# Kernel tuning notes

Measured on AMD Instinct MI355X. Metric: run time of the kernel, lower is better.

Reference implementation:

```python
import jax, jax.numpy as jnp
import numpy as np

B, S, D, F = 4, 2048, 1024, 4096

def setup_inputs() -> dict:
    key = jax.random.key(0)
    ks = jax.random.split(key, 6)
    return {
        "x": jax.random.normal(ks[0], (B, S, D), jnp.float32),
        "Qw": jax.random.normal(ks[1], (D, D), jnp.float32) / 40,
        "Kw": jax.random.normal(ks[2], (D, D), jnp.float32) / 40,
        "Vw": jax.random.normal(ks[3], (D, D), jnp.float32) / 40,
        "w1": jax.random.normal(ks[4], (D, F), jnp.float32) / 40,
        "b1": jnp.zeros((F,), jnp.float32),
        "w2": jax.random.normal(ks[5], (F, D), jnp.float32) / 40,
        "b2": jnp.zeros((D,), jnp.float32),
        "gamma1": jnp.ones((D,), jnp.float32),
        "beta1": jnp.zeros((D,), jnp.float32),
        "gamma2": jnp.ones((D,), jnp.float32),
        "beta2": jnp.zeros((D,), jnp.float32),
    }

def _layernorm(x, gamma, beta):
    num = x - jnp.mean(x, axis=-1, keepdims=True)
    den = jnp.sqrt(jnp.var(x, axis=-1, keepdims=True) + 1e-05)
    return gamma * (num / den) + beta

def _attention(x, Qw, Kw, Vw):
    Q, K, V = x @ Qw, x @ Kw, x @ Vw
    d = x.shape[-1]
    s = x.shape[-2]
    mask = jnp.where(jnp.tril(jnp.ones((s, s))) == 0, -jnp.inf, 0.0)
    scores = Q @ jnp.swapaxes(K, -1, -2) / jnp.sqrt(d) + mask
    return jax.nn.softmax(scores, axis=-1) @ V

def reference(x, Qw, Kw, Vw, w1, b1, w2, b2, gamma1, beta1, gamma2, beta2):
    x = x + _attention(_layernorm(x, gamma1, beta1), Qw, Kw, Vw)
    h = _layernorm(x, gamma2, beta2)
    x = x + (jax.nn.relu(h @ w1 + b1) @ w2 + b2)
    return x
```

## Files before the change

### kernel.cpp

```cpp
#include <hip/hip_runtime.h>
#include <hip/hip_bf16.h>

#define B_ 4
#define S_ 2048
#define D_ 1024
#define F_ 4096

typedef short bf16x8 __attribute__((ext_vector_type(8)));
typedef float f32x4 __attribute__((ext_vector_type(4)));

static __device__ __forceinline__ unsigned short f2bf(float f) {
    union { float f; unsigned int u; } v; v.f = f;
    unsigned int u = v.u + 0x7FFF + ((v.u >> 16) & 1);
    return (unsigned short)(u >> 16);
}
static __device__ __forceinline__ float bf2f(unsigned short u) {
    union { unsigned int u; float f; } v; v.u = ((unsigned int)u) << 16;
    return v.f;
}

typedef const __attribute__((address_space(1))) unsigned int* gp_t;
typedef __attribute__((address_space(3))) unsigned int* lp_t;
static __device__ __forceinline__ void gld16(const unsigned short* g, unsigned short* l) {
    __builtin_amdgcn_global_load_lds((gp_t)g, (lp_t)l, 16, 0, 0);
}

#define WAIT_VM8()   __builtin_amdgcn_s_waitcnt(0x0F78)
#define WAIT_VM6()   __builtin_amdgcn_s_waitcnt(0x0F76)
#define WAIT_VM0()   __builtin_amdgcn_s_waitcnt(0x0F70)
#define WAIT_LGKM0() __builtin_amdgcn_s_waitcnt(0xC07F)

__global__ __launch_bounds__(256) void k_transpose_f32_bf16(
    const float* __restrict__ in, unsigned short* __restrict__ out, int R, int C) {
    __shared__ float t[32][33];
    int c0 = blockIdx.x * 32, r0 = blockIdx.y * 32;
    int x = threadIdx.x, y = threadIdx.y;
#pragma unroll
    for (int i = 0; i < 4; i++)
        t[y + 8 * i][x] = in[(size_t)(r0 + y + 8 * i) * C + c0 + x];
    __syncthreads();
#pragma unroll
    for (int i = 0; i < 4; i++)
        out[(size_t)(c0 + y + 8 * i) * R + r0 + x] = f2bf(t[x][y + 8 * i]);
}

__global__ __launch_bounds__(256) void k_transpose_w3(
    const float* __restrict__ Qw, const float* __restrict__ Kw, const float* __restrict__ Vw,
    unsigned short* __restrict__ out) {
    __shared__ float t[32][33];
    int z = blockIdx.z;
    const float* in = (z == 0) ? Qw : (z == 1) ? Kw : Vw;
    out += (size_t)z * D_ * D_;
    int c0 = blockIdx.x * 32, r0 = blockIdx.y * 32;
    int x = threadIdx.x, y = threadIdx.y;
#pragma unroll
    for (int i = 0; i < 4; i++)
        t[y + 8 * i][x] = in[(size_t)(r0 + y + 8 * i) * D_ + c0 + x];
    __syncthreads();
#pragma unroll
    for (int i = 0; i < 4; i++)
        out[(size_t)(c0 + y + 8 * i) * D_ + r0 + x] = f2bf(t[x][y + 8 * i]);
}

__global__ __launch_bounds__(256) void k_layernorm(
    const float* __restrict__ x, const float* __restrict__ gamma,
    const float* __restrict__ beta, unsigned short* __restrict__ out) {
    int row = blockIdx.x;
    int t = threadIdx.x;
    const float* xr = x + (size_t)row * D_;
    float4 v = ((const float4*)xr)[t];
    float s = v.x + v.y + v.z + v.w;
    float q = v.x * v.x + v.y * v.y + v.z * v.z + v.w * v.w;
#pragma unroll
    for (int off = 32; off; off >>= 1) {
        s += __shfl_down(s, off);
        q += __shfl_down(q, off);
    }
    __shared__ float ls[4], lq[4];
    int wv = t >> 6;
    if ((t & 63) == 0) { ls[wv] = s; lq[wv] = q; }
    __syncthreads();
    if (t == 0) {
        float S = ls[0] + ls[1] + ls[2] + ls[3];
        float Q = lq[0] + lq[1] + lq[2] + lq[3];
        float mean = S * (1.0f / D_);
        float var = Q * (1.0f / D_) - mean * mean;
        ls[0] = mean; lq[0] = rsqrtf(var + 1e-5f);
    }
    __syncthreads();
    float mean = ls[0], rstd = lq[0];
    float4 g = ((const float4*)gamma)[t];
    float4 b = ((const float4*)beta)[t];
    ushort4 o;
    o.x = f2bf(g.x * (v.x - mean) * rstd + b.x);
    o.y = f2bf(g.y * (v.y - mean) * rstd + b.y);
    o.z = f2bf(g.z * (v.z - mean) * rstd + b.z);
    o.w = f2bf(g.w * (v.w - mean) * rstd + b.w);
    ((ushort4*)(out + (size_t)row * D_))[t] = o;
}

__global__ __launch_bounds__(256) void k_softmax(unsigned short* __restrict__ sp) {
    int r = blockIdx.x;
    int i = r & (S_ - 1);
    unsigned short* row = sp + (size_t)r * S_;
    int t = threadIdx.x;
    int valid = i + 1;
    int wlim = (valid + 127) & ~127;
    bf16x8 v8 = {};
    if (t * 8 < valid) v8 = *(const bf16x8*)(row + t * 8);
    float vals[8];
    float mx = -1e30f;
#pragma unroll
    for (int k = 0; k < 8; k++) {
        int j = t * 8 + k;
        vals[k] = (j < valid) ? bf2f((unsigned short)v8[k]) : -1e30f;
        mx = fmaxf(mx, vals[k]);
    }
#pragma unroll
    for (int off = 32; off; off >>= 1) mx = fmaxf(mx, __shfl_xor(mx, off));
    __shared__ float red[4];
    if ((t & 63) == 0) red[t >> 6] = mx;
    __syncthreads();
    mx = fmaxf(fmaxf(red[0], red[1]), fmaxf(red[2], red[3]));
    __syncthreads();
    float e[8];
    float sum = 0.f;
#pragma unroll
    for (int k = 0; k < 8; k++) {
        int j = t * 8 + k;
        e[k] = (j < valid) ? __expf(vals[k] - mx) : 0.f;
        sum += e[k];
    }
#pragma unroll
    for (int off = 32; off; off >>= 1) sum += __shfl_xor(sum, off);
    if ((t & 63) == 0) red[t >> 6] = sum;
    __syncthreads();
    sum = red[0] + red[1] + red[2] + red[3];
    float inv = 1.0f / sum;
    if (t * 8 < wlim) {
        bf16x8 o8;
#pragma unroll
        for (int k = 0; k < 8; k++) o8[k] = (short)f2bf(e[k] * inv);
        *(bf16x8*)(row + t * 8) = o8;
    }
}

template <int EPI>
__global__ __launch_bounds__(256) void k_gemm_bt(
    const unsigned short* __restrict__ A, const unsigned short* __restrict__ Bt,
    void* __restrict__ Cv, const float* __restrict__ bias, const float* __restrict__ res,
    int K, int lda, int ldb, int ldc,
    long long sA, long long sB, long long sC, float scale, int klimit, int swz) {
    int bn, bm, z;
    if (swz > 0) {
        int GN = gridDim.x, GM = gridDim.y;
        int L = blockIdx.x + GN * (blockIdx.y + GM * blockIdx.z);
        int rows = gridDim.y * gridDim.z;
        int xcd = L & 7;
        int s = L >> 3;
        int bng = GN / swz;
        int rpg = rows * swz / 8;
        int xg = xcd % swz, yg = xcd / swz;
        int bnl = s % bng;
        int rl = s / bng;
        int row = yg * rpg + rl;
        bn = xg * bng + bnl;
        bm = row % GM;
        z = row / GM;
    } else {
        bn = blockIdx.x; bm = blockIdx.y; z = blockIdx.z;
    }
    if (EPI == 1 && bn > bm) return;
    A += (long long)z * sA;
    Bt += (long long)z * sB;
    long long coff = (long long)z * sC;
    float* Cf = (float*)Cv;
    unsigned short* Cb = (unsigned short*)Cv;

    __shared__ unsigned short As[2][2][128 * 32];
    __shared__ unsigned short Bs[2][2][128 * 32];

    int t = threadIdx.x;
    int l = t & 63, w = t >> 6;
    int wm = (w & 1) * 64, wn = (w >> 1) * 64;
    int lr = l & 15, lq = l >> 4;

    f32x4 acc[4][4];
#pragma unroll
    for (int i = 0; i < 4; i++)
#pragma unroll
        for (int j = 0; j < 4; j++) acc[i][j] = (f32x4){0.f, 0.f, 0.f, 0.f};

    int kend = K;
    if (klimit) { int ke = (bm + 1) * 128; kend = ke < K ? ke : K; }

    int sr = l >> 2;
    int sc = (l & 3) * 8;
    const unsigned short* gA0 = A + (size_t)(bm * 128 + w * 32 + sr) * lda + sc;
    const unsigned short* gA1 = gA0 + (size_t)16 * lda;
    const unsigned short* gB0 = Bt + (size_t)(bn * 128 + w * 32 + sr) * ldb + sc;
    const unsigned short* gB1 = gB0 + (size_t)16 * ldb;

    auto stage = [&](int buf, int k0) {
#pragma unroll
        for (int kc = 0; kc < 2; kc++) {
            int kk = k0 + kc * 32;
            gld16(gA0 + kk, &As[buf][kc][(w * 32) * 32]);
            gld16(gA1 + kk, &As[buf][kc][(w * 32 + 16) * 32]);
            gld16(gB0 + kk, &Bs[buf][kc][(w * 32) * 32]);
            gld16(gB1 + kk, &Bs[buf][kc][(w * 32 + 16) * 32]);
        }
    };

    int NB = kend >> 6;
    stage(0, 0);
    for (int it = 0; it < NB; it++) {
        int cur = it & 1;
        if (it + 1 < NB) {
            stage(1 - cur, (it + 1) * 64);
            WAIT_VM8();
        } else {
            WAIT_VM0();
        }
        __builtin_amdgcn_s_barrier();
#pragma unroll
        for (int kc = 0; kc < 2; kc++) {
            bf16x8 af[4], bf[4];
#pragma unroll
            for (int i = 0; i < 4; i++)
                af[i] = *(const bf16x8*)(&As[cur][kc][(wm + i * 16 + lr) * 32 + lq * 8]);
#pragma unroll
            for (int j = 0; j < 4; j++)
                bf[j] = *(const bf16x8*)(&Bs[cur][kc][(wn + j * 16 + lr) * 32 + lq * 8]);
#pragma unroll
            for (int i = 0; i < 4; i++)
#pragma unroll
                for (int j = 0; j < 4; j++)
                    acc[i][j] = __builtin_amdgcn_mfma_f32_16x16x32_bf16(af[i], bf[j], acc[i][j], 0, 0, 0);
        }
        __builtin_amdgcn_s_barrier();
    }

#pragma unroll
    for (int i = 0; i < 4; i++) {
        int mbase = bm * 128 + wm + i * 16 + lq * 4;
#pragma unroll
        for (int j = 0; j < 4; j++) {
            int n = bn * 128 + wn + j * 16 + lr;
#pragma unroll
            for (int r = 0; r < 4; r++) {
                int m = mbase + r;
                float v = acc[i][j][r];
                long long idx = coff + (long long)m * ldc + n;
                if (EPI == 0) {
                    Cb[idx] = f2bf(v);
                } else if (EPI == 1) {
                    Cb[idx] = f2bf(v * scale);
                } else if (EPI == 2) {
                    Cf[idx] = v + res[idx];
                } else if (EPI == 3) {
                    float u = v + bias[n];
                    Cb[idx] = f2bf(u > 0.f ? u : 0.f);
                } else {
                    Cf[idx] = v + bias[n] + res[idx];
                }
            }
        }
    }
}

template <int EPI>
__global__ __launch_bounds__(512, 2) void k_gemm256(
    const unsigned short* __restrict__ A, const unsigned short* __restrict__ Bt,
    void* __restrict__ Cv, const float* __restrict__ bias, const float* __restrict__ res,
    int K, int lda, int ldb, int ldc,
    long long sA, long long sB, long long sC, float scale, int klimit) {
    int bn = blockIdx.x, bm = blockIdx.y, z = blockIdx.z;
    if (EPI == 1 && bn > bm) return;
    A += (long long)z * sA;
    Bt += (long long)z * sB;
    long long coff = (long long)z * sC;
    float* Cf = (float*)Cv;
    unsigned short* Cb = (unsigned short*)Cv;

    __shared__ unsigned short As[2][2][128 * 64];
    __shared__ unsigned short Bs[2][2][128 * 64];

    int t = threadIdx.x;
    int l = t & 63, w = t >> 6;
    int wmh = w >> 2;
    int wnh = (w >> 1) & 1;
    int bnl = (w & 1) * 64;
    int lr = l & 15, lq = l >> 4;
    int rx = (lr & 7) << 3;
    int c0 = lq * 8;

    f32x4 acc[8][4];
#pragma unroll
    for (int i = 0; i < 8; i++)
#pragma unroll
        for (int j = 0; j < 4; j++) acc[i][j] = (f32x4){0.f, 0.f, 0.f, 0.f};

    int kend = K;
    if (klimit) { int ke = (bm + 1) * 256; kend = ke < K ? ke : K; }
    int NB = kend >> 6;

    int grow = l >> 3;
    int gcol = ((l & 7) * 8) ^ (((l >> 3) & 7) << 3);
    const unsigned short* gA = A + (size_t)(bm * 256 + w * 16 + grow) * lda + gcol;
    const unsigned short* gB = Bt + (size_t)(bn * 256 + w * 16 + grow) * ldb + gcol;

    auto stageA = [&](int buf, int half, int k0) {
        const unsigned short* g = gA + (size_t)(half * 128) * lda + k0;
        unsigned short* s = &As[buf][half][(w * 16) * 64];
        gld16(g, s);
        gld16(g + (size_t)8 * lda, s + 8 * 64);
    };
    auto stageB = [&](int buf, int half, int k0) {
        const unsigned short* g = gB + (size_t)(half * 128) * ldb + k0;
        unsigned short* s = &Bs[buf][half][(w * 16) * 64];
        gld16(g, s);
        gld16(g + (size_t)8 * ldb, s + 8 * 64);
    };

    stageA(0, 0, 0); stageA(0, 1, 0);
    stageB(0, 0, 0); stageB(0, 1, 0);
    int kp = (NB > 1) ? 64 : 0;
    stageB(1, 0, kp); stageB(1, 1, kp); stageA(1, 0, kp);
    WAIT_VM6();
    __builtin_amdgcn_s_barrier();

    bf16x8 aF0[2][4], aF1[2][4], bF[2][4];

    for (int j = 0; j < NB; j++) {
        int b = j & 1;
        int k1 = ((j + 1 < NB) ? (j + 1) : (NB - 1)) << 6;
        int k2 = ((j + 2 < NB) ? (j + 2) : (NB - 1)) << 6;
        const unsigned short* Ah = &As[b][wmh][0];
        const unsigned short* Bh = &Bs[b][wnh][0];

#pragma unroll
        for (int kc = 0; kc < 2; kc++) {
#pragma unroll
            for (int f = 0; f < 4; f++)
                bF[kc][f] = *(const bf16x8*)(Bh + (bnl + f * 16 + lr) * 64 + ((kc * 32 + c0) ^ rx));
#pragma unroll
            for (int f = 0; f < 4; f++)
                aF0[kc][f] = *(const bf16x8*)(Ah + (f * 16 + lr) * 64 + ((kc * 32 + c0) ^ rx));
        }
        stageA(b ^ 1, 1, k1);
        __builtin_amdgcn_s_barrier();
        __builtin_amdgcn_s_setprio(1);
#pragma unroll
        for (int kc = 0; kc < 2; kc++)
#pragma unroll
            for (int i = 0; i < 4; i++)
#pragma unroll
                for (int jn = 0; jn < 2; jn++)
                    acc[i][jn] = __builtin_amdgcn_mfma_f32_16x16x32_bf16(
                        aF0[kc][i], bF[kc][jn], acc[i][jn], 0, 0, 0);
        __builtin_amdgcn_s_setprio(0);
        __builtin_amdgcn_s_barrier();

#pragma unroll
        for (int kc = 0; kc < 2; kc++)
#pragma unroll
            for (int f = 0; f < 4; f++)
                aF1[kc][f] = *(const bf16x8*)(Ah + (64 + f * 16 + lr) * 64 + ((kc * 32 + c0) ^ rx));
        stageB(b, 0, k2);
        __builtin_amdgcn_s_barrier();
        __builtin_amdgcn_s_setprio(1);
#pragma unroll
        for (int kc = 0; kc < 2; kc++)
#pragma unroll
            for (int i = 0; i < 4; i++)
#pragma unroll
                for (int jn = 0; jn < 2; jn++)
                    acc[4 + i][jn] = __builtin_amdgcn_mfma_f32_16x16x32_bf16(
                        aF1[kc][i], bF[kc][jn], acc[4 + i][jn], 0, 0, 0);
        __builtin_amdgcn_s_setprio(0);
        __builtin_amdgcn_s_barrier();

        stageB(b, 1, k2);
        __builtin_amdgcn_s_barrier();
        __builtin_amdgcn_s_setprio(1);
#pragma unroll
        for (int kc = 0; kc < 2; kc++)
#pragma unroll
            for (int i = 0; i < 4; i++)
#pragma unroll
                for (int jn = 0; jn < 2; jn++)
                    acc[4 + i][2 + jn] = __builtin_amdgcn_mfma_f32_16x16x32_bf16(
                        aF1[kc][i], bF[kc][2 + jn], acc[4 + i][2 + jn], 0, 0, 0);
        __builtin_amdgcn_s_setprio(0);
        __builtin_amdgcn_s_barrier();

        stageA(b, 0, k2);
        WAIT_VM6();
        __builtin_amdgcn_s_barrier();
        __builtin_amdgcn_s_setprio(1);
#pragma unroll
        for (int kc = 0; kc < 2; kc++)
#pragma unroll
            for (int i = 0; i < 4; i++)
#pragma unroll
                for (int jn = 0; jn < 2; jn++)
                    acc[i][2 + jn] = __builtin_amdgcn_mfma_f32_16x16x32_bf16(
                        aF0[kc][i], bF[kc][2 + jn], acc[i][2 + jn], 0, 0, 0);
        __builtin_amdgcn_s_setprio(0);
        __builtin_amdgcn_s_barrier();
    }
    WAIT_VM0();

    if (EPI == 6 && bn >= 8) {
        __builtin_amdgcn_s_barrier();
        unsigned short* T = (w < 4) ? (unsigned short*)As + (size_t)w * 8192
                                    : (unsigned short*)Bs + (size_t)(w - 4) * 8192;
#pragma unroll
        for (int i = 0; i < 8; i++)
#pragma unroll
            for (int jn = 0; jn < 4; jn++) {
                int nl = jn * 16 + lr;
                int ml = i * 16 + lq * 4;
                ushort4 o;
                o.x = f2bf(acc[i][jn][0]);
                o.y = f2bf(acc[i][jn][1]);
                o.z = f2bf(acc[i][jn][2]);
                o.w = f2bf(acc[i][jn][3]);
                *(ushort4*)&T[nl * 128 + (((ml & ~7) ^ ((nl & 7) << 3)) | (ml & 7))] = o;
            }
        WAIT_LGKM0();
        __builtin_amdgcn_s_barrier();
        unsigned short* VTp = (unsigned short*)(size_t)res;
        int batch = (bm * 256) >> 11;
        size_t mb0 = (size_t)((bm * 256) & 2047) + (size_t)wmh * 128;
        size_t nb0 = (size_t)(bn * 256 - 2048 + (w & 3) * 64);
        size_t vbase = (size_t)batch * D_ * S_ + mb0;
#pragma unroll
        for (int p = 0; p < 16; p++) {
            int nl = p * 4 + (l >> 4);
            int mo = (l & 15) * 8;
            bf16x8 v = *(const bf16x8*)&T[nl * 128 + (mo ^ ((nl & 7) << 3))];
            *(bf16x8*)(VTp + vbase + (nb0 + nl) * S_ + mo) = v;
        }
    } else {
#pragma unroll
        for (int i = 0; i < 8; i++) {
            int mbase = bm * 256 + wmh * 128 + i * 16 + lq * 4;
#pragma unroll
            for (int jn = 0; jn < 4; jn++) {
                int n = bn * 256 + (w & 3) * 64 + jn * 16 + lr;
#pragma unroll
                for (int r = 0; r < 4; r++) {
                    int m = mbase + r;
                    float v = acc[i][jn][r];
                    long long idx = coff + (long long)m * ldc + n;
                    if (EPI == 0 || EPI == 6) {
                        Cb[idx] = f2bf(v);
                    } else if (EPI == 1) {
                        Cb[idx] = f2bf(v * scale);
                    } else if (EPI == 2) {
                        Cf[idx] = v + res[idx];
                    } else if (EPI == 3) {
                        float u = v + bias[n];
                        Cb[idx] = f2bf(u > 0.f ? u : 0.f);
                    } else {
                        Cf[idx] = v + bias[n] + res[idx];
                    }
                }
            }
        }
    }
}

extern "C" void kernel_launch(void* const* d_in, const int* in_sizes, int n_in,
                              void* d_out, int out_size, void* d_ws, size_t ws_size,
                              hipStream_t stream) {
    const float* x      = (const float*)d_in[0];
    const float* Qw     = (const float*)d_in[1];
    const float* Kw     = (const float*)d_in[2];
    const float* Vw     = (const float*)d_in[3];
    const float* w1     = (const float*)d_in[4];
    const float* b1     = (const float*)d_in[5];
    const float* w2     = (const float*)d_in[6];
    const float* b2     = (const float*)d_in[7];
    const float* gamma1 = (const float*)d_in[8];
    const float* beta1  = (const float*)d_in[9];
    const float* gamma2 = (const float*)d_in[10];
    const float* beta2  = (const float*)d_in[11];
    float* out = (float*)d_out;

    char* ws = (char*)d_ws;
    size_t off = 0;
    auto alloc = [&](size_t bytes) -> void* {
        void* p = ws + off;
        off += (bytes + 255) & ~(size_t)255;
        return p;
    };
    const size_t MN = (size_t)B_ * S_ * D_;
    unsigned short* xn     = (unsigned short*)alloc(MN * 2);
    unsigned short* scoreP = (unsigned short*)alloc((size_t)B_ * S_ * S_ * 2);
    unsigned short* qkv    = (unsigned short*)alloc((size_t)B_ * S_ * 3072 * 2);
    unsigned short* VT     = (unsigned short*)alloc(MN * 2);
    unsigned short* QKVwT  = (unsigned short*)alloc((size_t)3 * D_ * D_ * 2);
    unsigned short* w1T    = (unsigned short*)alloc((size_t)D_ * F_ * 2);
    unsigned short* w2T    = (unsigned short*)alloc((size_t)F_ * D_ * 2);
    unsigned short* mid = qkv;

    dim3 tb(32, 8);
    k_transpose_w3<<<dim3(D_ / 32, D_ / 32, 3), tb, 0, stream>>>(Qw, Kw, Vw, QKVwT);
    k_transpose_f32_bf16<<<dim3(F_ / 32, D_ / 32), tb, 0, stream>>>(w1, w1T, D_, F_);
    k_transpose_f32_bf16<<<dim3(D_ / 32, F_ / 32), tb, 0, stream>>>(w2, w2T, F_, D_);

    k_layernorm<<<B_ * S_, 256, 0, stream>>>(x, gamma1, beta1, xn);

    const int Mtok = B_ * S_;
    k_gemm256<6><<<dim3(3072 / 256, Mtok / 256), 512, 0, stream>>>(
        xn, QKVwT, qkv, nullptr, (const float*)VT, D_, D_, D_, 3072, 0, 0, 0, 1.f, 0);

    k_gemm256<1><<<dim3(S_ / 256, S_ / 256, B_), 512, 0, stream>>>(
        qkv, qkv + 1024, scoreP, nullptr, nullptr, D_, 3072, 3072, S_,
        (long long)S_ * 3072, (long long)S_ * 3072, (long long)S_ * S_, 0.03125f, 0);

    k_softmax<<<B_ * S_, 256, 0, stream>>>(scoreP);

    k_gemm_bt<2><<<dim3(D_ / 128, S_ / 128, B_), 256, 0, stream>>>(
        scoreP, VT, out, nullptr, x, S_, S_, S_, D_,
        (long long)S_ * S_, (long long)D_ * S_, (long long)S_ * D_, 1.f, 1, 2);

    k_layernorm<<<B_ * S_, 256, 0, stream>>>(out, gamma2, beta2, xn);

    k_gemm256<3><<<dim3(F_ / 256, Mtok / 256), 512, 0, stream>>>(
        xn, w1T, mid, b1, nullptr, D_, D_, D_, F_, 0, 0, 0, 1.f, 0);

    k_gemm_bt<4><<<dim3(D_ / 128, Mtok / 128), 256, 0, stream>>>(
        mid, w2T, out, b2, out, F_, F_, F_, D_, 0, 0, 0, 1.f, 0, 2);
}
```

Baseline: 462.6 us.

## Add XCD-aware block swizzle to 256 GEMMs and merge weight transposes

```diff
diff --git a/kernel.cpp b/kernel.cpp
--- a/kernel.cpp
+++ b/kernel.cpp
@@ -30,10 +30,31 @@
 #define WAIT_VM0()   __builtin_amdgcn_s_waitcnt(0x0F70)
 #define WAIT_LGKM0() __builtin_amdgcn_s_waitcnt(0xC07F)
 
-__global__ __launch_bounds__(256) void k_transpose_f32_bf16(
-    const float* __restrict__ in, unsigned short* __restrict__ out, int R, int C) {
+__global__ __launch_bounds__(256) void k_transpose_weights(
+    const float* __restrict__ Qw, const float* __restrict__ Kw,
+    const float* __restrict__ Vw, const float* __restrict__ w1,
+    const float* __restrict__ w2, unsigned short* __restrict__ QKVwT,
+    unsigned short* __restrict__ w1T, unsigned short* __restrict__ w2T) {
     __shared__ float t[32][33];
-    int c0 = blockIdx.x * 32, r0 = blockIdx.y * 32;
+    int id = blockIdx.x;
+    const float* in;
+    unsigned short* out;
+    int R, C, bx, by;
+    if (id < 3072) {
+        int z = id >> 10, r = id & 1023;
+        in = (z == 0) ? Qw : (z == 1) ? Kw : Vw;
+        out = QKVwT + (size_t)z * D_ * D_;
+        R = D_; C = D_; bx = r & 31; by = r >> 5;
+    } else if (id < 7168) {
+        int r = id - 3072;
+        in = w1; out = w1T; R = D_; C = F_;
+        bx = r & 127; by = r >> 7;
+    } else {
+        int r = id - 7168;
+        in = w2; out = w2T; R = F_; C = D_;
+        bx = r & 31; by = r >> 5;
+    }
+    int c0 = bx * 32, r0 = by * 32;
     int x = threadIdx.x, y = threadIdx.y;
 #pragma unroll
     for (int i = 0; i < 4; i++)
@@ -42,24 +63,6 @@
 #pragma unroll
     for (int i = 0; i < 4; i++)
         out[(size_t)(c0 + y + 8 * i) * R + r0 + x] = f2bf(t[x][y + 8 * i]);
-}
-
-__global__ __launch_bounds__(256) void k_transpose_w3(
-    const float* __restrict__ Qw, const float* __restrict__ Kw, const float* __restrict__ Vw,
-    unsigned short* __restrict__ out) {
-    __shared__ float t[32][33];
-    int z = blockIdx.z;
-    const float* in = (z == 0) ? Qw : (z == 1) ? Kw : Vw;
-    out += (size_t)z * D_ * D_;
-    int c0 = blockIdx.x * 32, r0 = blockIdx.y * 32;
-    int x = threadIdx.x, y = threadIdx.y;
-#pragma unroll
-    for (int i = 0; i < 4; i++)
-        t[y + 8 * i][x] = in[(size_t)(r0 + y + 8 * i) * D_ + c0 + x];
-    __syncthreads();
-#pragma unroll
-    for (int i = 0; i < 4; i++)
-        out[(size_t)(c0 + y + 8 * i) * D_ + r0 + x] = f2bf(t[x][y + 8 * i]);
 }
 
 __global__ __launch_bounds__(256) void k_layernorm(
@@ -274,8 +277,26 @@
     const unsigned short* __restrict__ A, const unsigned short* __restrict__ Bt,
     void* __restrict__ Cv, const float* __restrict__ bias, const float* __restrict__ res,
     int K, int lda, int ldb, int ldc,
-    long long sA, long long sB, long long sC, float scale, int klimit) {
-    int bn = blockIdx.x, bm = blockIdx.y, z = blockIdx.z;
+    long long sA, long long sB, long long sC, float scale, int klimit, int swz) {
+    int bn, bm, z;
+    if (swz > 0) {
+        int GN = gridDim.x, GM = gridDim.y;
+        int L = blockIdx.x + GN * (blockIdx.y + GM * blockIdx.z);
+        int rows = gridDim.y * gridDim.z;
+        int xcd = L & 7;
+        int s = L >> 3;
+        int bng = GN / swz;
+        int rpg = rows * swz / 8;
+        int xg = xcd % swz, yg = xcd / swz;
+        int bnl = s % bng;
+        int rl = s / bng;
+        int row = yg * rpg + rl;
+        bn = xg * bng + bnl;
+        bm = row % GM;
+        z = row / GM;
+    } else {
+        bn = blockIdx.x; bm = blockIdx.y; z = blockIdx.z;
+    }
     if (EPI == 1 && bn > bm) return;
     A += (long long)z * sA;
     Bt += (long long)z * sB;
@@ -290,7 +311,7 @@
     int l = t & 63, w = t >> 6;
     int wmh = w >> 2;
     int wnh = (w >> 1) & 1;
-    int bnl = (w & 1) * 64;
+    int bnl2 = (w & 1) * 64;
     int lr = l & 15, lq = l >> 4;
     int rx = (lr & 7) << 3;
     int c0 = lq * 8;
@@ -343,7 +364,7 @@
         for (int kc = 0; kc < 2; kc++) {
 #pragma unroll
             for (int f = 0; f < 4; f++)
-                bF[kc][f] = *(const bf16x8*)(Bh + (bnl + f * 16 + lr) * 64 + ((kc * 32 + c0) ^ rx));
+                bF[kc][f] = *(const bf16x8*)(Bh + (bnl2 + f * 16 + lr) * 64 + ((kc * 32 + c0) ^ rx));
 #pragma unroll
             for (int f = 0; f < 4; f++)
                 aF0[kc][f] = *(const bf16x8*)(Ah + (f * 16 + lr) * 64 + ((kc * 32 + c0) ^ rx));
@@ -507,20 +528,18 @@
     unsigned short* w2T    = (unsigned short*)alloc((size_t)F_ * D_ * 2);
     unsigned short* mid = qkv;
 
-    dim3 tb(32, 8);
-    k_transpose_w3<<<dim3(D_ / 32, D_ / 32, 3), tb, 0, stream>>>(Qw, Kw, Vw, QKVwT);
-    k_transpose_f32_bf16<<<dim3(F_ / 32, D_ / 32), tb, 0, stream>>>(w1, w1T, D_, F_);
-    k_transpose_f32_bf16<<<dim3(D_ / 32, F_ / 32), tb, 0, stream>>>(w2, w2T, F_, D_);
+    k_transpose_weights<<<11264, dim3(32, 8), 0, stream>>>(
+        Qw, Kw, Vw, w1, w2, QKVwT, w1T, w2T);
 
     k_layernorm<<<B_ * S_, 256, 0, stream>>>(x, gamma1, beta1, xn);
 
     const int Mtok = B_ * S_;
     k_gemm256<6><<<dim3(3072 / 256, Mtok / 256), 512, 0, stream>>>(
-        xn, QKVwT, qkv, nullptr, (const float*)VT, D_, D_, D_, 3072, 0, 0, 0, 1.f, 0);
+        xn, QKVwT, qkv, nullptr, (const float*)VT, D_, D_, D_, 3072, 0, 0, 0, 1.f, 0, 2);
 
     k_gemm256<1><<<dim3(S_ / 256, S_ / 256, B_), 512, 0, stream>>>(
         qkv, qkv + 1024, scoreP, nullptr, nullptr, D_, 3072, 3072, S_,
-        (long long)S_ * 3072, (long long)S_ * 3072, (long long)S_ * S_, 0.03125f, 0);
+        (long long)S_ * 3072, (long long)S_ * 3072, (long long)S_ * S_, 0.03125f, 0, 0);
 
     k_softmax<<<B_ * S_, 256, 0, stream>>>(scoreP);
 
@@ -531,7 +550,7 @@
     k_layernorm<<<B_ * S_, 256, 0, stream>>>(out, gamma2, beta2, xn);
 
     k_gemm256<3><<<dim3(F_ / 256, Mtok / 256), 512, 0, stream>>>(
-        xn, w1T, mid, b1, nullptr, D_, D_, D_, F_, 0, 0, 0, 1.f, 0);
+        xn, w1T, mid, b1, nullptr, D_, D_, D_, F_, 0, 0, 0, 1.f, 0, 2);
 
     k_gemm_bt<4><<<dim3(D_ / 128, Mtok / 128), 256, 0, stream>>>(
         mid, w2T, out, b2, out, F_, F_, F_, D_, 0, 0, 0, 1.f, 0, 2);
```

Result: no change. 457.5 us (-1.1%).
